# Optimization experiments

Measured on AMD Instinct MI355X. Metric: run time of the kernel, lower is better.

Reference implementation:

```python
import jax, jax.numpy as jnp
import numpy as np

SIGMA = 0.3
EPS = 1e-8  # torch CosineSimilarity eps
LOG_SQRT_2PI = float(0.5 * np.log(2.0 * np.pi))


def setup_inputs() -> dict:
    key = jax.random.key(0)
    k1, k2 = jax.random.split(key)
    Ex = jax.random.normal(k1, (8192, 256), dtype=jnp.float32)
    Ey = jax.random.normal(k2, (8192, 256), dtype=jnp.float32)
    return {"Ex": Ex, "Ey": Ey}


def reference(Ex, Ey):
    # cosine similarity: normalize rows (clamped norms), then dot -> [n, m]
    xn = Ex / jnp.maximum(jnp.linalg.norm(Ex, axis=-1, keepdims=True), EPS)
    yn = Ey / jnp.maximum(jnp.linalg.norm(Ey, axis=-1, keepdims=True), EPS)
    M = jnp.einsum('nd,md->nm', xn, yn)
    # Normal(loc=1, scale=sigma).log_prob
    z = (M - 1.0) / SIGMA
    logp = -0.5 * z * z - jnp.log(jnp.asarray(SIGMA, M.dtype)) - LOG_SQRT_2PI
    # C = -(exp(logp) * logp); row-wise min over y-tokens -> [n]
    C = -jnp.exp(logp) * logp
    return jnp.min(C, axis=-1)
```

## Files before the change

kernel.cpp:

```cpp
#include <hip/hip_runtime.h>
#include <hip/hip_bf16.h>

typedef unsigned short u16;
typedef __attribute__((ext_vector_type(8))) short short8;
typedef __attribute__((ext_vector_type(4))) float floatx4;

#define NROWS 8192
#define DIM 256

__device__ __forceinline__ void atomicMinFloat(float* addr, float val) {
    if (val >= 0.0f) {
        atomicMin((int*)addr, __float_as_int(val));
    } else {
        atomicMax((unsigned int*)addr, __float_as_uint(val));
    }
}

__device__ __forceinline__ u16 f32_to_bf16_rne(float x) {
    unsigned int u = __float_as_uint(x);
    unsigned int r = (u + 0x7fffu + ((u >> 16) & 1u)) >> 16;
    return (u16)r;
}

__device__ __forceinline__ float c_of_m(float m) {
    const float INV_SIG = 1.0f / 0.3f;
    const float KC = 0.28503427f;
    float z = (m - 1.0f) * INV_SIG;
    float logp = fmaf(-0.5f * z, z, KC);
    return -logp * __expf(logp);
}

__device__ __forceinline__ void load16(const u16* g, u16* l) {
    __builtin_amdgcn_global_load_lds(
        (__attribute__((address_space(1))) void*)g,
        (__attribute__((address_space(3))) void*)l, 16, 0, 0);
}

__global__ __launch_bounds__(256) void normalize_kernel(const float* __restrict__ Ex,
                                                        const float* __restrict__ Ey,
                                                        u16* __restrict__ Xs,
                                                        u16* __restrict__ Ys,
                                                        float* __restrict__ out) {
    const int t = threadIdx.x;
    const int ln = t & 63;
    const int row = blockIdx.x * 4 + (t >> 6);
    const float* src = (blockIdx.y == 0) ? Ex : Ey;
    u16* dst = (blockIdx.y == 0) ? Xs : Ys;

    float4 v = *(const float4*)(src + (size_t)row * DIM + ln * 4);
    float s = fmaf(v.x, v.x, fmaf(v.y, v.y, fmaf(v.z, v.z, v.w * v.w)));
    #pragma unroll
    for (int m = 32; m >= 1; m >>= 1) s += __shfl_xor(s, m, 64);
    float inv = 1.0f / fmaxf(sqrtf(s), 1e-8f);

    ushort4 o;
    o.x = f32_to_bf16_rne(v.x * inv);
    o.y = f32_to_bf16_rne(v.y * inv);
    o.z = f32_to_bf16_rne(v.z * inv);
    o.w = f32_to_bf16_rne(v.w * inv);

    const int p = row >> 4;
    const int lm = row & 15;
    const int kt = ln >> 3;
    const int lq = (ln >> 1) & 3;
    const int j4 = (ln & 1) * 4;
    const size_t off = ((size_t)((p * 8 + kt) * 64 + lq * 16 + lm)) * 8 + j4;
    *(ushort4*)(dst + off) = o;

    if (blockIdx.y == 0 && ln == 0) out[row] = __uint_as_float(0x7f800000u);
}

__global__ void __launch_bounds__(512, 2)
gemm_min_kernel(const u16* __restrict__ Xs,
                const u16* __restrict__ Ys,
                float* __restrict__ out) {
    __shared__ u16 Bs[2][32 * 512];

    const int tid = threadIdx.x;
    const int w = tid >> 6;
    const int lane = tid & 63;
    const int lq = lane >> 4;
    const int lm = lane & 15;

    const int b = blockIdx.x;
    const int rowStart = (b & 15) * 512;
    const int rowPan0 = (b & 15) * 32 + w * 4;
    const u16* ybase = Ys + (size_t)((b >> 4) * 32) * 4096;

    auto stageB = [&](int buf, const u16* yb) {
        #pragma unroll
        for (int i = 0; i < 4; ++i) {
            const int u = w * 4 + i;
            load16(yb + (u >> 3) * 4096 + (u & 7) * 512 + lane * 8,
                   &Bs[buf][u * 512]);
        }
    };

    short8 a[4][8];
    auto loadA = [&](int kt) {
        #pragma unroll
        for (int rg = 0; rg < 4; ++rg)
            a[rg][kt] = *(const short8*)(
                Xs + ((size_t)(rowPan0 + rg) * 8 + kt) * 512 + lane * 8);
    };

    floatx4 mn4[4], mx4[4];
    #pragma unroll
    for (int rg = 0; rg < 4; ++rg) {
        mn4[rg] = (floatx4){3.4e38f, 3.4e38f, 3.4e38f, 3.4e38f};
        mx4[rg] = (floatx4){-3.4e38f, -3.4e38f, -3.4e38f, -3.4e38f};
    }

    floatx4 acc[4][4];
    auto zeroAcc = [&]() {
        #pragma unroll
        for (int i = 0; i < 4; ++i)
            #pragma unroll
            for (int j = 0; j < 4; ++j)
                acc[i][j] = (floatx4){0.0f, 0.0f, 0.0f, 0.0f};
    };
    auto compute = [&](int buf) {
        #pragma unroll
        for (int kt = 0; kt < 8; ++kt) {
            short8 bf[4];
            #pragma unroll
            for (int cg = 0; cg < 4; ++cg)
                bf[cg] = *(const short8*)(&Bs[buf][(cg * 8 + kt) * 512 + lane * 8]);
            #pragma unroll
            for (int cg = 0; cg < 4; ++cg)
                #pragma unroll
                for (int rg = 0; rg < 4; ++rg)
                    acc[rg][cg] = __builtin_amdgcn_mfma_f32_16x16x32_bf16(
                        a[rg][kt], bf[cg], acc[rg][cg], 0, 0, 0);
        }
    };
    auto fold = [&]() {
        #pragma unroll
        for (int rg = 0; rg < 4; ++rg)
            #pragma unroll
            for (int cg = 0; cg < 4; ++cg)
                #pragma unroll
                for (int r = 0; r < 4; ++r) {
                    float m = acc[rg][cg][r];
                    mn4[rg][r] = fminf(mn4[rg][r], m);
                    mx4[rg][r] = fmaxf(mx4[rg][r], m);
                }
    };

    stageB(0, ybase);
    loadA(0);
    loadA(1);
    __syncthreads();
    stageB(1, ybase + 16384);
    loadA(2); loadA(3); loadA(4); loadA(5); loadA(6); loadA(7);
    zeroAcc();
    compute(0);
    fold();
    ybase += 16384;

    #pragma unroll 1
    for (int ct = 1; ct < 8; ++ct) {
        const int buf = ct & 1;
        zeroAcc();
        __syncthreads();
        if (ct < 7)
            stageB(buf ^ 1, ybase + 16384);
        compute(buf);
        fold();
        ybase += 16384;
    }

    #pragma unroll
    for (int rg = 0; rg < 4; ++rg) {
        #pragma unroll
        for (int r = 0; r < 4; ++r) {
            float mn = mn4[rg][r];
            float mx = mx4[rg][r];
            #pragma unroll
            for (int mofs = 1; mofs < 16; mofs <<= 1) {
                mn = fminf(mn, __shfl_xor(mn, mofs, 64));
                mx = fmaxf(mx, __shfl_xor(mx, mofs, 64));
            }
            if (lm == 0) {
                float cmin = fminf(c_of_m(mn), c_of_m(mx));
                int row = rowStart + w * 64 + rg * 16 + lq * 4 + r;
                atomicMinFloat(&out[row], cmin);
            }
        }
    }
}

extern "C" void kernel_launch(void* const* d_in, const int* in_sizes, int n_in,
                              void* d_out, int out_size, void* d_ws, size_t ws_size,
                              hipStream_t stream) {
    const float* Ex = (const float*)d_in[0];
    const float* Ey = (const float*)d_in[1];
    float* out = (float*)d_out;
    u16* Xs = (u16*)d_ws;
    u16* Ys = Xs + (size_t)NROWS * DIM;

    hipLaunchKernelGGL(normalize_kernel, dim3(NROWS / 4, 2), dim3(256), 0, stream,
                       Ex, Ey, Xs, Ys, out);
    hipLaunchKernelGGL(gemm_min_kernel, dim3(16 * 16), dim3(512), 0, stream,
                       Xs, Ys, out);
}
```

Measured before the change: 94.98 us.

## Stage B tiles through registers interleaved with MFMA halves instead of direct-to-LDS loads

Replaces the global_load_lds direct-to-LDS staging of the B tile with ordinary vector global loads into registers, followed by explicit LDS stores. The loads and stores are split into two halves and interleaved with two half-K MFMA compute phases, so global latency is hidden behind matrix work. This gives the compiler explicit control over the overlap. In exchange it costs extra VGPRs and LDS write instructions, which may raise register pressure at the 512x2 launch bounds.

```diff
diff --git a/kernel.cpp b/kernel.cpp
--- a/kernel.cpp
+++ b/kernel.cpp
@@ -28,12 +28,6 @@
     float z = (m - 1.0f) * INV_SIG;
     float logp = fmaf(-0.5f * z, z, KC);
     return -logp * __expf(logp);
-}
-
-__device__ __forceinline__ void load16(const u16* g, u16* l) {
-    __builtin_amdgcn_global_load_lds(
-        (__attribute__((address_space(1))) void*)g,
-        (__attribute__((address_space(3))) void*)l, 16, 0, 0);
 }
 
 __global__ __launch_bounds__(256) void normalize_kernel(const float* __restrict__ Ex,
@@ -87,12 +81,18 @@
     const int rowPan0 = (b & 15) * 32 + w * 4;
     const u16* ybase = Ys + (size_t)((b >> 4) * 32) * 4096;
 
-    auto stageB = [&](int buf, const u16* yb) {
-        #pragma unroll
-        for (int i = 0; i < 4; ++i) {
-            const int u = w * 4 + i;
-            load16(yb + (u >> 3) * 4096 + (u & 7) * 512 + lane * 8,
-                   &Bs[buf][u * 512]);
+    auto loadB2 = [&](uint4 (&r)[2], const u16* yb, int i0) {
+        #pragma unroll
+        for (int i = 0; i < 2; ++i) {
+            const int u = w * 4 + i0 + i;
+            r[i] = *(const uint4*)(yb + (u >> 3) * 4096 + (u & 7) * 512 + lane * 8);
+        }
+    };
+    auto writeB2 = [&](int buf, const uint4 (&r)[2], int i0) {
+        #pragma unroll
+        for (int i = 0; i < 2; ++i) {
+            const int u = w * 4 + i0 + i;
+            *(uint4*)(&Bs[buf][u * 512 + lane * 8]) = r[i];
         }
     };
 
@@ -119,9 +119,10 @@
             for (int j = 0; j < 4; ++j)
                 acc[i][j] = (floatx4){0.0f, 0.0f, 0.0f, 0.0f};
     };
-    auto compute = [&](int buf) {
-        #pragma unroll
-        for (int kt = 0; kt < 8; ++kt) {
+    auto computeHalf = [&](int buf, int h) {
+        #pragma unroll
+        for (int k = 0; k < 4; ++k) {
+            const int kt = h * 4 + k;
             short8 bf[4];
             #pragma unroll
             for (int cg = 0; cg < 4; ++cg)
@@ -147,25 +148,45 @@
                 }
     };
 
-    stageB(0, ybase);
-    loadA(0);
-    loadA(1);
-    __syncthreads();
-    stageB(1, ybase + 16384);
-    loadA(2); loadA(3); loadA(4); loadA(5); loadA(6); loadA(7);
-    zeroAcc();
-    compute(0);
-    fold();
-    ybase += 16384;
+    {
+        uint4 ra[2], rc[2];
+        loadB2(ra, ybase, 0);
+        loadB2(rc, ybase, 2);
+        loadA(0);
+        loadA(1);
+        writeB2(0, ra, 0);
+        writeB2(0, rc, 2);
+        __syncthreads();
+
+        loadB2(ra, ybase + 16384, 0);
+        loadA(2); loadA(3); loadA(4); loadA(5); loadA(6); loadA(7);
+        zeroAcc();
+        computeHalf(0, 0);
+        writeB2(1, ra, 0);
+        loadB2(rc, ybase + 16384, 2);
+        computeHalf(0, 1);
+        writeB2(1, rc, 2);
+        fold();
+        ybase += 16384;
+    }
 
     #pragma unroll 1
     for (int ct = 1; ct < 8; ++ct) {
         const int buf = ct & 1;
         zeroAcc();
         __syncthreads();
-        if (ct < 7)
-            stageB(buf ^ 1, ybase + 16384);
-        compute(buf);
+        if (ct < 7) {
+            uint4 ra[2], rc[2];
+            loadB2(ra, ybase + 16384, 0);
+            computeHalf(buf, 0);
+            writeB2(buf ^ 1, ra, 0);
+            loadB2(rc, ybase + 16384, 2);
+            computeHalf(buf, 1);
+            writeB2(buf ^ 1, rc, 2);
+        } else {
+            computeHalf(buf, 0);
+            computeHalf(buf, 1);
+        }
         fold();
         ybase += 16384;
     }
```

New measurement: 104.7 us. 10.2% more time.
